# Kernel optimization log

Hardware: AMD Instinct MI355X
Metric: run time of the kernel (lower is better)

## Reference

```python
import math
import jax, jax.numpy as jnp
import numpy as np

B, T, D, H = 2, 2048, 768, 12
DH = D // H
EPS = 1e-5


def setup_inputs() -> dict:
    key = jax.random.key(0)
    ks = jax.random.split(key, 8)
    s = 0.02
    x = jax.random.normal(ks[0], (B, T, D), dtype=jnp.float32)
    lengths = jax.random.randint(ks[1], (B,), T // 2, T + 1)
    lengths = lengths.at[0].set(T)  # ensure max(lengths)==T (static shape)
    return {
        'x': x,
        'lengths': lengths,
        'w_qkv': jax.random.normal(ks[2], (D, 3 * D), dtype=jnp.float32) * s,
        'b_qkv': jnp.zeros((3 * D,), jnp.float32),
        'w_proj': jax.random.normal(ks[3], (D, D), dtype=jnp.float32) * s,
        'b_proj': jnp.zeros((D,), jnp.float32),
        'ln1_g': jnp.ones((D,), jnp.float32),
        'ln1_b': jnp.zeros((D,), jnp.float32),
        'w_fc': jax.random.normal(ks[4], (D, 4 * D), dtype=jnp.float32) * s,
        'b_fc': jnp.zeros((4 * D,), jnp.float32),
        'w_out': jax.random.normal(ks[5], (4 * D, D), dtype=jnp.float32) * s,
        'b_out': jnp.zeros((D,), jnp.float32),
        'ln2_g': jnp.ones((D,), jnp.float32),
        'ln2_b': jnp.zeros((D,), jnp.float32),
    }


def _gelu(x):
    c = math.sqrt(2.0 / math.pi)
    return 0.5 * x * (1.0 + jnp.tanh(c * (x + 0.044715 * x * x * x)))


def _layernorm(x, g, b):
    mu = jnp.mean(x, axis=-1, keepdims=True)
    var = jnp.mean(jnp.square(x - mu), axis=-1, keepdims=True)
    return (x - mu) * jax.lax.rsqrt(var + EPS) * g + b


def _block(x, lengths, w_qkv, b_qkv, w_proj, b_proj, ln1_g, ln1_b,
           w_fc, b_fc, w_out, b_out, ln2_g, ln2_b):
    dt = x.dtype
    # [B, T] validity mask from ragged lengths
    pos = jnp.arange(T)
    mask = (pos[None, :] < lengths[:, None]).astype(dt)

    # --- SeqMultiHeadAttention (scale=False) ---
    qkv = x @ w_qkv + b_qkv  # [B, T, 3D]
    q, k, v = jnp.split(qkv, 3, axis=-1)

    def split_heads(t):  # [B,T,D] -> [B,H,T,DH]
        return t.reshape(B, T, H, DH).transpose(0, 2, 1, 3)

    q, k, v = split_heads(q), split_heads(k), split_heads(v)
    w = jnp.einsum('bhqd,bhkd->bhqk', q, k)  # [B,H,T,T]
    amask = (mask[:, None, :, None] * mask[:, None, None, :])  # [B,1,T,T]
    w = w * amask + (-1e9) * (1.0 - amask)
    w = jax.nn.softmax(w, axis=-1) * amask
    a = jnp.einsum('bhqk,bhkd->bhqd', w, v)  # [B,H,T,DH]
    a = a.transpose(0, 2, 1, 3).reshape(B, T, D)
    a = a @ w_proj + b_proj

    # --- SeqLayerNorm 1: pack/unpack == per-position LN, padding zeroed ---
    n = _layernorm(x + a, ln1_g, ln1_b) * mask[..., None]

    # --- MLP (gelu) ---
    m = _gelu(n @ w_fc + b_fc) @ w_out + b_out

    # --- SeqLayerNorm 2 ---
    h = _layernorm(n + m, ln2_g, ln2_b) * mask[..., None]
    return h


def reference(x, lengths, w_qkv, b_qkv, w_proj, b_proj, ln1_g, ln1_b,
              w_fc, b_fc, w_out, b_out, ln2_g, ln2_b):
    return _block(x, lengths, w_qkv, b_qkv, w_proj, b_proj, ln1_g, ln1_b,
                  w_fc, b_fc, w_out, b_out, ln2_g, ln2_b)
```

## Files before the change

### kernel.cpp

```cpp
#include <hip/hip_runtime.h>
#include <hip/hip_bf16.h>
#include <math.h>

constexpr int Bc  = 2;
constexpr int Tc  = 2048;
constexpr int Dc  = 768;
constexpr int Hc  = 12;
constexpr int DHc = 64;
constexpr int M_ROWS = Bc * Tc;
constexpr int D3  = 3 * Dc;
constexpr int D4  = 4 * Dc;

typedef __attribute__((ext_vector_type(8))) short short8;
typedef __attribute__((ext_vector_type(4))) float f32x4;

__device__ __forceinline__ unsigned short f2bf(float v) {
    union { __hip_bfloat16 b; unsigned short u; } cv;
    cv.b = __float2bfloat16(v);
    return cv.u;
}
__device__ __forceinline__ float bf2f(unsigned short u) {
    union { __hip_bfloat16 b; unsigned short u; } cv;
    cv.u = u;
    return __bfloat162float(cv.b);
}
__device__ __forceinline__ void bsplit(float v, unsigned short& h, unsigned short& l) {
    h = f2bf(v);
    l = f2bf(v - bf2f(h));
}

__device__ __forceinline__ float gelu_f(float x) {
    const float c = 0.79788456080286535588f;
    return 0.5f * x * (1.0f + tanhf(c * (x + 0.044715f * x * x * x)));
}

__device__ __forceinline__ void glds16(const unsigned short* g, unsigned short* l) {
    __builtin_amdgcn_global_load_lds(
        (const __attribute__((address_space(1))) void*)g,
        (__attribute__((address_space(3))) void*)l, 16, 0, 0);
}

__device__ __forceinline__ void tcast8(
    const float* __restrict__ w, int ldw,
    unsigned short* __restrict__ th, int K, int N, int idx)
{
    const int n  = idx % N;
    const int k0 = (idx / N) * 8;
    unsigned short hv[8];
#pragma unroll
    for (int j = 0; j < 8; ++j)
        hv[j] = f2bf(w[(size_t)(k0 + j) * ldw + n]);
    const size_t o = (size_t)n * K + k0;
    *(ushort4*)(th + o)     = make_ushort4(hv[0], hv[1], hv[2], hv[3]);
    *(ushort4*)(th + o + 4) = make_ushort4(hv[4], hv[5], hv[6], hv[7]);
}

__global__ __launch_bounds__(256) void prepare_kernel(
    const float* __restrict__ x,
    const float* __restrict__ w_qkv, const float* __restrict__ w_proj,
    const float* __restrict__ w_fc,  const float* __restrict__ w_out,
    unsigned short* __restrict__ xh,
    unsigned short* __restrict__ wqkvT, unsigned short* __restrict__ wprojT,
    unsigned short* __restrict__ wfcT,  unsigned short* __restrict__ woutT)
{
    int id = blockIdx.x * 256 + threadIdx.x;
    if (id < 786432) {
        const float4 v = *(const float4*)(x + (size_t)id * 4);
        *(ushort4*)(xh + (size_t)id * 4) =
            make_ushort4(f2bf(v.x), f2bf(v.y), f2bf(v.z), f2bf(v.w));
        return;
    }
    id -= 786432;
    if (id < 221184) { tcast8(w_qkv, D3, wqkvT, Dc, D3, id); return; }
    id -= 221184;
    if (id < 73728)  { tcast8(w_proj, Dc, wprojT, Dc, Dc, id); return; }
    id -= 73728;
    if (id < 294912) { tcast8(w_fc, D4, wfcT, Dc, D4, id); return; }
    id -= 294912;
    tcast8(w_out, Dc, woutT, D4, Dc, id);
}

template <int TM, int MODE>
__global__ __launch_bounds__(256) void gemm_bf16(
    const unsigned short* __restrict__ A,
    const unsigned short* __restrict__ B,
    const float* __restrict__ bias,
    float* __restrict__ C, unsigned short* __restrict__ Cb,
    int M, int N, int K)
{
    constexpr int MT = TM / 32;
    __shared__ unsigned short Ash[TM * 64];
    __shared__ unsigned short Bsh[128 * 64];

    const int tid  = threadIdx.x;
    const int n0   = blockIdx.x * 128;
    const int m0   = blockIdx.y * TM;
    const int wave = tid >> 6;
    const int lane = tid & 63;
    const int wm   = (wave >> 1) * (TM / 2);
    const int wn   = (wave & 1) * 64;
    const int lrow = lane & 15;
    const int quad = lane >> 4;
    const int swz  = lrow & 7;

    f32x4 acc[MT][4];
    const f32x4 zero = {0.f, 0.f, 0.f, 0.f};
#pragma unroll
    for (int i = 0; i < MT; ++i)
#pragma unroll
        for (int j = 0; j < 4; ++j) acc[i][j] = zero;

    const int l8r  = lane >> 3;
    const int csel = ((lane & 7) ^ l8r) * 8;

    for (int ks = 0; ks < K; ks += 64) {
        __syncthreads();
#pragma unroll
        for (int j = 0; j < TM / 32; ++j) {
            const int rbase = wave * (TM / 4) + j * 8;
            const size_t g = (size_t)(m0 + rbase + l8r) * K + ks + csel;
            glds16(A + g, &Ash[rbase * 64]);
        }
#pragma unroll
        for (int j = 0; j < 4; ++j) {
            const int rbase = wave * 32 + j * 8;
            const size_t g = (size_t)(n0 + rbase + l8r) * K + ks + csel;
            glds16(B + g, &Bsh[rbase * 64]);
        }
        __syncthreads();

#pragma unroll
        for (int kk = 0; kk < 2; ++kk) {
            short8 fa[MT], fb[4];
            const int cl = kk * 4 + quad;
            const int pc = (cl ^ swz) * 8;
#pragma unroll
            for (int t = 0; t < MT; ++t)
                fa[t] = *(const short8*)&Ash[(wm + t * 16 + lrow) * 64 + pc];
#pragma unroll
            for (int t = 0; t < 4; ++t)
                fb[t] = *(const short8*)&Bsh[(wn + t * 16 + lrow) * 64 + pc];
#pragma unroll
            for (int mt = 0; mt < MT; ++mt)
#pragma unroll
                for (int nt = 0; nt < 4; ++nt)
                    acc[mt][nt] = __builtin_amdgcn_mfma_f32_16x16x32_bf16(
                        fa[mt], fb[nt], acc[mt][nt], 0, 0, 0);
        }
    }

#pragma unroll
    for (int mt = 0; mt < MT; ++mt) {
        const int rowb = m0 + wm + mt * 16 + quad * 4;
#pragma unroll
        for (int nt = 0; nt < 4; ++nt) {
            const int col = n0 + wn + nt * 16 + lrow;
            const float bv = bias[col];
#pragma unroll
            for (int r = 0; r < 4; ++r) {
                const size_t ci = (size_t)(rowb + r) * N + col;
                if (MODE == 0) {
                    C[ci] = acc[mt][nt][r] + bv;
                } else if (MODE == 1) {
                    Cb[ci] = f2bf(gelu_f(acc[mt][nt][r] + bv));
                } else {
                    Cb[ci] = f2bf(acc[mt][nt][r] + bv);
                }
            }
        }
    }
}

constexpr int KS  = 72;
constexpr int PS2 = 72;

__global__ __launch_bounds__(256) void flash_attn_bf16(
    const unsigned short* __restrict__ qkv,
    const int* __restrict__ lengths,
    unsigned short* __restrict__ oh)
{
    __shared__ unsigned short Kh[64 * KS];
    __shared__ unsigned short Vt[64 * KS];
    __shared__ unsigned short PfU[64 * PS2];

    const int tid  = threadIdx.x;
    const int wave = tid >> 6;
    const int lane = tid & 63;
    const int m    = lane & 15;
    const int quad = lane >> 4;

    const int nqt = Tc / 64;
    const int qt  = blockIdx.x % nqt;
    const int bh  = blockIdx.x / nqt;
    const int hh  = bh % Hc;
    const int b   = bh / Hc;
    const int len = lengths[b];
    const int q0  = qt * 64;
    const size_t rs = (size_t)D3;
    const unsigned short* base = qkv + (size_t)b * Tc * rs;
    const int qcol = hh * DHc;
    const int kcol = Dc + hh * DHc;
    const int vcol = 2 * Dc + hh * DHc;

    if (q0 >= len) {
#pragma unroll
        for (int r = 0; r < 4; ++r) {
            const int qrow = q0 + wave * 16 + quad * 4 + r;
            const size_t ob = (size_t)(b * Tc + qrow) * Dc + hh * DHc + m;
#pragma unroll
            for (int nt = 0; nt < 4; ++nt) oh[ob + nt * 16] = 0;
        }
        return;
    }

    const int ktEnd = (min(len, Tc) + 63) >> 6;

    short8 Qf[2];
#pragma unroll
    for (int ch = 0; ch < 2; ++ch) {
        const size_t ga = (size_t)(q0 + wave * 16 + m) * rs + qcol + ch * 32 + quad * 8;
        const short8 q8 = *(const short8*)&base[ga];
        short8 qs;
#pragma unroll
        for (int j = 0; j < 8; ++j)
            qs[j] = (short)f2bf(bf2f((unsigned short)q8[j]) * 1.44269504088896f);
        Qf[ch] = qs;
    }

    f32x4 Oacc[4];
    const f32x4 zero = {0.f, 0.f, 0.f, 0.f};
#pragma unroll
    for (int nt = 0; nt < 4; ++nt) Oacc[nt] = zero;
    float lrow[4] = {0.f, 0.f, 0.f, 0.f};

    const int kr0 = tid >> 3,          kc0 = (tid & 7) * 8;
    const int kr1 = (tid + 256) >> 3,  kc1 = ((tid + 256) & 7) * 8;
    const int pk  = (tid >> 4) * 4;
    const int pd  = (tid & 15) * 4;
    const int vswz = ((pk >> 3) ^ ((pd >> 2) & 7)) * 8 + (pk & 7);

    short8  pK0, pK1;
    ushort4 pV0, pV1, pV2, pV3;
    {
        pK0 = *(const short8*)&base[(size_t)kr0 * rs + kcol + kc0];
        pK1 = *(const short8*)&base[(size_t)kr1 * rs + kcol + kc1];
        pV0 = *(const ushort4*)&base[(size_t)(pk + 0) * rs + vcol + pd];
        pV1 = *(const ushort4*)&base[(size_t)(pk + 1) * rs + vcol + pd];
        pV2 = *(const ushort4*)&base[(size_t)(pk + 2) * rs + vcol + pd];
        pV3 = *(const ushort4*)&base[(size_t)(pk + 3) * rs + vcol + pd];
    }

    for (int kt = 0; kt < ktEnd; ++kt) {
        const int kbase = kt * 64;
        __syncthreads();

        *(short8*)&Kh[kr0 * KS + kc0] = pK0;
        *(short8*)&Kh[kr1 * KS + kc1] = pK1;
        *(ushort4*)&Vt[(pd + 0) * KS + vswz] = make_ushort4(pV0.x, pV1.x, pV2.x, pV3.x);
        *(ushort4*)&Vt[(pd + 1) * KS + vswz] = make_ushort4(pV0.y, pV1.y, pV2.y, pV3.y);
        *(ushort4*)&Vt[(pd + 2) * KS + vswz] = make_ushort4(pV0.z, pV1.z, pV2.z, pV3.z);
        *(ushort4*)&Vt[(pd + 3) * KS + vswz] = make_ushort4(pV0.w, pV1.w, pV2.w, pV3.w);
        __syncthreads();

        if (kt + 1 < ktEnd) {
            const int nb = kbase + 64;
            pK0 = *(const short8*)&base[(size_t)(nb + kr0) * rs + kcol + kc0];
            pK1 = *(const short8*)&base[(size_t)(nb + kr1) * rs + kcol + kc1];
            pV0 = *(const ushort4*)&base[(size_t)(nb + pk + 0) * rs + vcol + pd];
            pV1 = *(const ushort4*)&base[(size_t)(nb + pk + 1) * rs + vcol + pd];
            pV2 = *(const ushort4*)&base[(size_t)(nb + pk + 2) * rs + vcol + pd];
            pV3 = *(const ushort4*)&base[(size_t)(nb + pk + 3) * rs + vcol + pd];
        }

        f32x4 S4[4];
#pragma unroll
        for (int nt = 0; nt < 4; ++nt) S4[nt] = zero;
#pragma unroll
        for (int ch = 0; ch < 2; ++ch)
#pragma unroll
            for (int nt = 0; nt < 4; ++nt) {
                const short8 k8 = *(const short8*)&Kh[(nt * 16 + m) * KS + ch * 32 + quad * 8];
                S4[nt] = __builtin_amdgcn_mfma_f32_16x16x32_bf16(Qf[ch], k8, S4[nt], 0, 0, 0);
            }

        if (kbase + 64 > len) {
#pragma unroll
            for (int nt = 0; nt < 4; ++nt)
                if (kbase + nt * 16 + m >= len) {
#pragma unroll
                    for (int r = 0; r < 4; ++r) S4[nt][r] = -1e30f;
                }
        }

#pragma unroll
        for (int nt = 0; nt < 4; ++nt)
#pragma unroll
            for (int r = 0; r < 4; ++r) {
                const float p = __builtin_amdgcn_exp2f(S4[nt][r]);
                lrow[r] += p;
                PfU[(wave * 16 + quad * 4 + r) * PS2 + nt * 16 + m] = f2bf(p);
            }

#pragma unroll
        for (int ch = 0; ch < 2; ++ch) {
            const short8 P8 = *(const short8*)&PfU[(wave * 16 + m) * PS2 + ch * 32 + quad * 8];
#pragma unroll
            for (int nt = 0; nt < 4; ++nt) {
                const int pchunk = ((ch * 4 + quad) ^ ((nt * 4 + (m >> 2)) & 7)) * 8;
                const short8 v8 = *(const short8*)&Vt[(nt * 16 + m) * KS + pchunk];
                Oacc[nt] = __builtin_amdgcn_mfma_f32_16x16x32_bf16(P8, v8, Oacc[nt], 0, 0, 0);
            }
        }
    }

#pragma unroll
    for (int r = 0; r < 4; ++r) {
#pragma unroll
        for (int sh = 8; sh >= 1; sh >>= 1)
            lrow[r] += __shfl_xor(lrow[r], sh);
    }

#pragma unroll
    for (int r = 0; r < 4; ++r) {
        const int qrow = q0 + wave * 16 + quad * 4 + r;
        const size_t ob = (size_t)(b * Tc + qrow) * Dc + hh * DHc + m;
        if (qrow < len) {
            const float inv = 1.0f / lrow[r];
#pragma unroll
            for (int nt = 0; nt < 4; ++nt)
                oh[ob + nt * 16] = f2bf(Oacc[nt][r] * inv);
        } else {
#pragma unroll
            for (int nt = 0; nt < 4; ++nt)
                oh[ob + nt * 16] = 0;
        }
    }
}

__global__ __launch_bounds__(256) void ln_split_kernel(
    const float* __restrict__ X, const float* __restrict__ Y,
    const float* __restrict__ g, const float* __restrict__ beta,
    const int* __restrict__ lengths,
    unsigned short* __restrict__ outh, unsigned short* __restrict__ outl)
{
    __shared__ float red[4];
    const int row = blockIdx.x;
    const int b = row / Tc, t = row % Tc;
    const int len = lengths[b];
    const size_t basei = (size_t)row * Dc;
    const int tid = threadIdx.x;

    if (t >= len) {
        for (int j = tid; j < Dc; j += 256) { outh[basei + j] = 0; outl[basei + j] = 0; }
        return;
    }

    float v[3];
    float s = 0.f;
#pragma unroll
    for (int j = 0; j < 3; ++j) {
        int idx = tid + j * 256;
        v[j] = X[basei + idx] + Y[basei + idx];
        s += v[j];
    }
    const int lane = tid % 64, wid = tid / 64;
#pragma unroll
    for (int sh = 32; sh >= 1; sh >>= 1) s += __shfl_xor(s, sh);
    if (lane == 0) red[wid] = s;
    __syncthreads();
    s = red[0] + red[1] + red[2] + red[3];
    const float mu = s * (1.0f / Dc);

    float vs = 0.f;
#pragma unroll
    for (int j = 0; j < 3; ++j) { float dv = v[j] - mu; vs += dv * dv; }
    __syncthreads();
#pragma unroll
    for (int sh = 32; sh >= 1; sh >>= 1) vs += __shfl_xor(vs, sh);
    if (lane == 0) red[wid] = vs;
    __syncthreads();
    vs = red[0] + red[1] + red[2] + red[3];
    const float rstd = rsqrtf(vs * (1.0f / Dc) + 1e-5f);

#pragma unroll
    for (int j = 0; j < 3; ++j) {
        int idx = tid + j * 256;
        const float ov = (v[j] - mu) * rstd * g[idx] + beta[idx];
        unsigned short hh, ll;
        bsplit(ov, hh, ll);
        outh[basei + idx] = hh;
        outl[basei + idx] = ll;
    }
}

__global__ __launch_bounds__(256) void ln2_kernel(
    const unsigned short* __restrict__ Xh, const unsigned short* __restrict__ Xl,
    const float* Y,
    const float* __restrict__ g, const float* __restrict__ beta,
    const int* __restrict__ lengths, float* out)
{
    __shared__ float red[4];
    const int row = blockIdx.x;
    const int b = row / Tc, t = row % Tc;
    const int len = lengths[b];
    const size_t basei = (size_t)row * Dc;
    const int tid = threadIdx.x;

    if (t >= len) {
        for (int j = tid; j < Dc; j += 256) out[basei + j] = 0.f;
        return;
    }

    float v[3];
    float s = 0.f;
#pragma unroll
    for (int j = 0; j < 3; ++j) {
        int idx = tid + j * 256;
        v[j] = bf2f(Xh[basei + idx]) + bf2f(Xl[basei + idx]) + Y[basei + idx];
        s += v[j];
    }
    const int lane = tid % 64, wid = tid / 64;
#pragma unroll
    for (int sh = 32; sh >= 1; sh >>= 1) s += __shfl_xor(s, sh);
    if (lane == 0) red[wid] = s;
    __syncthreads();
    s = red[0] + red[1] + red[2] + red[3];
    const float mu = s * (1.0f / Dc);

    float vs = 0.f;
#pragma unroll
    for (int j = 0; j < 3; ++j) { float dv = v[j] - mu; vs += dv * dv; }
    __syncthreads();
#pragma unroll
    for (int sh = 32; sh >= 1; sh >>= 1) vs += __shfl_xor(vs, sh);
    if (lane == 0) red[wid] = vs;
    __syncthreads();
    vs = red[0] + red[1] + red[2] + red[3];
    const float rstd = rsqrtf(vs * (1.0f / Dc) + 1e-5f);

#pragma unroll
    for (int j = 0; j < 3; ++j) {
        int idx = tid + j * 256;
        out[basei + idx] = (v[j] - mu) * rstd * g[idx] + beta[idx];
    }
}

extern "C" void kernel_launch(void* const* d_in, const int* in_sizes, int n_in,
                              void* d_out, int out_size, void* d_ws, size_t ws_size,
                              hipStream_t stream)
{
    const float* x      = (const float*)d_in[0];
    const int*   lens   = (const int*)  d_in[1];
    const float* w_qkv  = (const float*)d_in[2];
    const float* b_qkv  = (const float*)d_in[3];
    const float* w_proj = (const float*)d_in[4];
    const float* b_proj = (const float*)d_in[5];
    const float* ln1_g  = (const float*)d_in[6];
    const float* ln1_b  = (const float*)d_in[7];
    const float* w_fc   = (const float*)d_in[8];
    const float* b_fc   = (const float*)d_in[9];
    const float* w_out  = (const float*)d_in[10];
    const float* b_out  = (const float*)d_in[11];
    const float* ln2_g  = (const float*)d_in[12];
    const float* ln2_b  = (const float*)d_in[13];

    if (ws_size < 51904512) return;

    char* ws = (char*)d_ws;
    unsigned short* qkvh  = (unsigned short*)(ws + 0);
    unsigned short* xh    = (unsigned short*)(ws + 18874368);
    unsigned short* ah    = xh;
    float*          projo = (float*)(ws + 0);
    unsigned short* fH    = (unsigned short*)(ws + 0);
    unsigned short* nh    = (unsigned short*)(ws + 25165824);
    unsigned short* nl    = (unsigned short*)(ws + 31457280);
    unsigned short* wqkvT = (unsigned short*)(ws + 37748736);
    unsigned short* wprojT= (unsigned short*)(ws + 41287680);
    unsigned short* wfcT  = (unsigned short*)(ws + 42467328);
    unsigned short* woutT = (unsigned short*)(ws + 47185920);
    float*          mbuf  = (float*)d_out;

    const dim3 blk(256);

    prepare_kernel<<<dim3(6528), blk, 0, stream>>>(
        x, w_qkv, w_proj, w_fc, w_out, xh, wqkvT, wprojT, wfcT, woutT);

    gemm_bf16<128, 3><<<dim3(D3 / 128, M_ROWS / 128), blk, 0, stream>>>(
        xh, wqkvT, b_qkv, nullptr, qkvh, M_ROWS, D3, Dc);

    flash_attn_bf16<<<dim3(Bc * Hc * (Tc / 64)), blk, 0, stream>>>(qkvh, lens, ah);

    gemm_bf16<64, 0><<<dim3(Dc / 128, M_ROWS / 64), blk, 0, stream>>>(
        ah, wprojT, b_proj, projo, nullptr, M_ROWS, Dc, Dc);

    ln_split_kernel<<<dim3(M_ROWS), blk, 0, stream>>>(x, projo, ln1_g, ln1_b, lens, nh, nl);

    gemm_bf16<128, 1><<<dim3(D4 / 128, M_ROWS / 128), blk, 0, stream>>>(
        nh, wfcT, b_fc, nullptr, fH, M_ROWS, D4, Dc);

    gemm_bf16<64, 0><<<dim3(Dc / 128, M_ROWS / 64), blk, 0, stream>>>(
        fH, woutT, b_out, mbuf, nullptr, M_ROWS, Dc, D4);

    ln2_kernel<<<dim3(M_ROWS), blk, 0, stream>>>(nh, nl, mbuf, ln2_g, ln2_b, lens,
                                                 (float*)d_out);
}
```

Measured before the change: 313.0 us.

## Double-buffer LDS tiles in bf16 GEMM to overlap global loads with MFMA

The bf16 GEMM kernel now keeps two LDS buffers for the A and B tiles. It issues the direct global-to-LDS loads for the next K step before running the MFMAs on the current buffer, with one barrier per iteration instead of two. The goal is to hide global memory latency behind matrix-core work. In exchange, shared memory use per block doubles, which can lower occupancy. Correctness also depends on the barrier waiting for the outstanding LDS-targeted loads.

```diff
diff --git a/kernel.cpp b/kernel.cpp
--- a/kernel.cpp
+++ b/kernel.cpp
@@ -89,8 +89,8 @@
     int M, int N, int K)
 {
     constexpr int MT = TM / 32;
-    __shared__ unsigned short Ash[TM * 64];
-    __shared__ unsigned short Bsh[128 * 64];
+    __shared__ unsigned short Ash[2][TM * 64];
+    __shared__ unsigned short Bsh[2][128 * 64];
 
     const int tid  = threadIdx.x;
     const int n0   = blockIdx.x * 128;
@@ -113,21 +113,38 @@
     const int l8r  = lane >> 3;
     const int csel = ((lane & 7) ^ l8r) * 8;
 
-    for (int ks = 0; ks < K; ks += 64) {
-        __syncthreads();
-#pragma unroll
-        for (int j = 0; j < TM / 32; ++j) {
-            const int rbase = wave * (TM / 4) + j * 8;
-            const size_t g = (size_t)(m0 + rbase + l8r) * K + ks + csel;
-            glds16(A + g, &Ash[rbase * 64]);
-        }
-#pragma unroll
-        for (int j = 0; j < 4; ++j) {
-            const int rbase = wave * 32 + j * 8;
-            const size_t g = (size_t)(n0 + rbase + l8r) * K + ks + csel;
-            glds16(B + g, &Bsh[rbase * 64]);
-        }
-        __syncthreads();
+    const int nsteps = K >> 6;
+
+#pragma unroll
+    for (int j = 0; j < TM / 32; ++j) {
+        const int rbase = wave * (TM / 4) + j * 8;
+        glds16(A + (size_t)(m0 + rbase + l8r) * K + csel, &Ash[0][rbase * 64]);
+    }
+#pragma unroll
+    for (int j = 0; j < 4; ++j) {
+        const int rbase = wave * 32 + j * 8;
+        glds16(B + (size_t)(n0 + rbase + l8r) * K + csel, &Bsh[0][rbase * 64]);
+    }
+    asm volatile("s_waitcnt vmcnt(0)" ::: "memory");
+    __syncthreads();
+
+    int cur = 0;
+    for (int s = 0; s < nsteps; ++s) {
+        if (s + 1 < nsteps) {
+            const int ksn = (s + 1) << 6;
+#pragma unroll
+            for (int j = 0; j < TM / 32; ++j) {
+                const int rbase = wave * (TM / 4) + j * 8;
+                glds16(A + (size_t)(m0 + rbase + l8r) * K + ksn + csel,
+                       &Ash[cur ^ 1][rbase * 64]);
+            }
+#pragma unroll
+            for (int j = 0; j < 4; ++j) {
+                const int rbase = wave * 32 + j * 8;
+                glds16(B + (size_t)(n0 + rbase + l8r) * K + ksn + csel,
+                       &Bsh[cur ^ 1][rbase * 64]);
+            }
+        }
 
 #pragma unroll
         for (int kk = 0; kk < 2; ++kk) {
@@ -136,10 +153,10 @@
             const int pc = (cl ^ swz) * 8;
 #pragma unroll
             for (int t = 0; t < MT; ++t)
-                fa[t] = *(const short8*)&Ash[(wm + t * 16 + lrow) * 64 + pc];
+                fa[t] = *(const short8*)&Ash[cur][(wm + t * 16 + lrow) * 64 + pc];
 #pragma unroll
             for (int t = 0; t < 4; ++t)
-                fb[t] = *(const short8*)&Bsh[(wn + t * 16 + lrow) * 64 + pc];
+                fb[t] = *(const short8*)&Bsh[cur][(wn + t * 16 + lrow) * 64 + pc];
 #pragma unroll
             for (int mt = 0; mt < MT; ++mt)
 #pragma unroll
@@ -147,6 +164,9 @@
                     acc[mt][nt] = __builtin_amdgcn_mfma_f32_16x16x32_bf16(
                         fa[mt], fb[nt], acc[mt][nt], 0, 0, 0);
         }
+
+        __syncthreads();
+        cur ^= 1;
     }
 
 #pragma unroll
```

Result: slower. 327.6 us (+4.7%).

## Add 256x256 double-buffered bf16 GEMM for QKV and FC projections

Applied to the files above, without the earlier changes.

Introduces a new 512-thread GEMM kernel with 256x256 output tiles, double-buffered LDS staging via direct global-to-LDS loads, an XOR-swizzled shared layout and an XCD-aware block index remap. It replaces the 128x128 GEMM for the QKV and FC1 (GELU) projections. The aim is more operand reuse per tile, overlap of loads with MFMA work, and better L2 locality per XCD. In exchange it uses 128KB of LDS and large accumulator register arrays, which limits occupancy. The grids are small (144 and 192 blocks on a 256-CU device), which may leave CUs idle.

```diff
diff --git a/kernel.cpp b/kernel.cpp
--- a/kernel.cpp
+++ b/kernel.cpp
@@ -78,6 +78,111 @@
     if (id < 294912) { tcast8(w_fc, D4, wfcT, Dc, D4, id); return; }
     id -= 294912;
     tcast8(w_out, Dc, woutT, D4, Dc, id);
+}
+
+template <int MODE>
+__global__ __launch_bounds__(512) void gemm256_bf16(
+    const unsigned short* __restrict__ A,
+    const unsigned short* __restrict__ B,
+    const float* __restrict__ bias,
+    float* __restrict__ C, unsigned short* __restrict__ Cb,
+    int N, int K)
+{
+    __shared__ unsigned short Ash[2][256 * 64];
+    __shared__ unsigned short Bsh[2][256 * 64];
+
+    const int tid  = threadIdx.x;
+    const int wave = tid >> 6;
+    const int lane = tid & 63;
+
+    const int nper = gridDim.x >> 3;
+    const int gid  = (blockIdx.x & 7) * nper + (blockIdx.x >> 3);
+    const int bx   = gid / 16;
+    const int by   = gid % 16;
+    const int m0 = by * 256, n0 = bx * 256;
+
+    const int wm   = (wave >> 2) * 128;
+    const int wn   = (wave & 3) * 64;
+    const int lrow = lane & 15;
+    const int quad = lane >> 4;
+    const int swz  = lrow & 7;
+
+    f32x4 acc[8][4];
+    const f32x4 zero = {0.f, 0.f, 0.f, 0.f};
+#pragma unroll
+    for (int i = 0; i < 8; ++i)
+#pragma unroll
+        for (int j = 0; j < 4; ++j) acc[i][j] = zero;
+
+    const int l8r  = lane >> 3;
+    const int csel = ((lane & 7) ^ l8r) * 8;
+
+    const int nsteps = K >> 6;
+
+    auto stage = [&](int t, int b) {
+        const int ks = t << 6;
+#pragma unroll
+        for (int j = 0; j < 4; ++j) {
+            const int rbase = wave * 32 + j * 8;
+            glds16(A + (size_t)(m0 + rbase + l8r) * K + ks + csel,
+                   &Ash[b][rbase * 64]);
+        }
+#pragma unroll
+        for (int j = 0; j < 4; ++j) {
+            const int rbase = wave * 32 + j * 8;
+            glds16(B + (size_t)(n0 + rbase + l8r) * K + ks + csel,
+                   &Bsh[b][rbase * 64]);
+        }
+    };
+
+    stage(0, 0);
+    __syncthreads();
+
+    int cur = 0;
+    for (int s = 0; s < nsteps; ++s) {
+        if (s + 1 < nsteps) stage(s + 1, cur ^ 1);
+
+#pragma unroll
+        for (int kk = 0; kk < 2; ++kk) {
+            const int pc = ((kk * 4 + quad) ^ swz) * 8;
+            short8 fb[4];
+#pragma unroll
+            for (int nt = 0; nt < 4; ++nt)
+                fb[nt] = *(const short8*)&Bsh[cur][(wn + nt * 16 + lrow) * 64 + pc];
+#pragma unroll
+            for (int mt = 0; mt < 8; ++mt) {
+                const short8 fa = *(const short8*)&Ash[cur][(wm + mt * 16 + lrow) * 64 + pc];
+#pragma unroll
+                for (int nt = 0; nt < 4; ++nt)
+                    acc[mt][nt] = __builtin_amdgcn_mfma_f32_16x16x32_bf16(
+                        fa, fb[nt], acc[mt][nt], 0, 0, 0);
+            }
+        }
+
+        __syncthreads();
+        cur ^= 1;
+    }
+
+#pragma unroll
+    for (int mt = 0; mt < 8; ++mt) {
+        const int rowb = m0 + wm + mt * 16 + quad * 4;
+#pragma unroll
+        for (int nt = 0; nt < 4; ++nt) {
+            const int col = n0 + wn + nt * 16 + lrow;
+            const float bv = bias[col];
+#pragma unroll
+            for (int r = 0; r < 4; ++r) {
+                const size_t ci = (size_t)(rowb + r) * N + col;
+                if (MODE == 0) {
+                    C[ci] = acc[mt][nt][r] + bv;
+                } else if (MODE == 1) {
+                    Cb[ci] = f2bf(gelu_f(acc[mt][nt][r] + bv));
+                } else {
+                    Cb[ci] = f2bf(acc[mt][nt][r] + bv);
+                }
+            }
+        }
+    }
 }
 
 template <int TM, int MODE>
@@ -485,8 +590,8 @@
     prepare_kernel<<<dim3(6528), blk, 0, stream>>>(
         x, w_qkv, w_proj, w_fc, w_out, xh, wqkvT, wprojT, wfcT, woutT);
 
-    gemm_bf16<128, 3><<<dim3(D3 / 128, M_ROWS / 128), blk, 0, stream>>>(
-        xh, wqkvT, b_qkv, nullptr, qkvh, M_ROWS, D3, Dc);
+    gemm256_bf16<3><<<dim3((D3 / 256) * 16), dim3(512), 0, stream>>>(
+        xh, wqkvT, b_qkv, nullptr, qkvh, D3, Dc);
 
     flash_attn_bf16<<<dim3(Bc * Hc * (Tc / 64)), blk, 0, stream>>>(qkvh, lens, ah);
 
@@ -495,8 +600,8 @@
 
     ln_split_kernel<<<dim3(M_ROWS), blk, 0, stream>>>(x, projo, ln1_g, ln1_b, lens, nh, nl);
 
-    gemm_bf16<128, 1><<<dim3(D4 / 128, M_ROWS / 128), blk, 0, stream>>>(
-        nh, wfcT, b_fc, nullptr, fH, M_ROWS, D4, Dc);
+    gemm256_bf16<1><<<dim3((D4 / 256) * 16), dim3(512), 0, stream>>>(
+        nh, wfcT, b_fc, nullptr, fH, D4, Dc);
 
     gemm_bf16<64, 0><<<dim3(Dc / 128, M_ROWS / 64), blk, 0, stream>>>(
         fH, woutT, b_out, mbuf, nullptr, M_ROWS, Dc, D4);
```

Result: slower. 323.4 us (+3.3%).

## Split attention over key range into two halves and combine partials

Applied to the files above, without the earlier changes.

The attention kernel now splits the key-tile loop into two halves run by separate blocks. Each block writes an unnormalized fp32 partial output and a row sum, and a new combine kernel adds them and normalizes to bf16. The goal is twice the grid parallelism on a GPU with many CUs, at the cost of extra fp32 global traffic and one more launch. The softmax appears to use a fixed max (no running max), which is what makes plain summing of the partials valid. The QKV and FC GEMMs also move to 64-row tiles for more blocks.

```diff
diff --git a/kernel.cpp b/kernel.cpp
--- a/kernel.cpp
+++ b/kernel.cpp
@@ -10,6 +10,7 @@
 constexpr int M_ROWS = Bc * Tc;
 constexpr int D3  = 3 * Dc;
 constexpr int D4  = 4 * Dc;
+constexpr int HT  = Bc * Hc * Tc;
 
 typedef __attribute__((ext_vector_type(8))) short short8;
 typedef __attribute__((ext_vector_type(4))) float f32x4;
@@ -174,10 +175,11 @@
 constexpr int KS  = 72;
 constexpr int PS2 = 72;
 
-__global__ __launch_bounds__(256) void flash_attn_bf16(
+__global__ __launch_bounds__(256) void flash_attn_split(
     const unsigned short* __restrict__ qkv,
     const int* __restrict__ lengths,
-    unsigned short* __restrict__ oh)
+    float* __restrict__ O0, float* __restrict__ O1,
+    float* __restrict__ lp)
 {
     __shared__ unsigned short Kh[64 * KS];
     __shared__ unsigned short Vt[64 * KS];
@@ -189,9 +191,12 @@
     const int m    = lane & 15;
     const int quad = lane >> 4;
 
-    const int nqt = Tc / 64;
-    const int qt  = blockIdx.x % nqt;
-    const int bh  = blockIdx.x / nqt;
+    const int nqt  = Tc / 64;
+    const int nblk = Bc * Hc * nqt;
+    const int half = blockIdx.x / nblk;
+    const int bid  = blockIdx.x % nblk;
+    const int qt  = bid % nqt;
+    const int bh  = bid / nqt;
     const int hh  = bh % Hc;
     const int b   = bh / Hc;
     const int len = lengths[b];
@@ -202,18 +207,24 @@
     const int kcol = Dc + hh * DHc;
     const int vcol = 2 * Dc + hh * DHc;
 
+    float* __restrict__ Op = half ? O1 : O0;
+    const int lbase = half * HT + (b * Hc + hh) * Tc;
+
     if (q0 >= len) {
 #pragma unroll
         for (int r = 0; r < 4; ++r) {
             const int qrow = q0 + wave * 16 + quad * 4 + r;
             const size_t ob = (size_t)(b * Tc + qrow) * Dc + hh * DHc + m;
 #pragma unroll
-            for (int nt = 0; nt < 4; ++nt) oh[ob + nt * 16] = 0;
+            for (int nt = 0; nt < 4; ++nt) Op[ob + nt * 16] = 0.f;
+            if (m == 0) lp[lbase + qrow] = 0.f;
         }
         return;
     }
 
     const int ktEnd = (min(len, Tc) + 63) >> 6;
+    const int kt0 = (half * ktEnd) >> 1;
+    const int kt1 = ((half + 1) * ktEnd) >> 1;
 
     short8 Qf[2];
 #pragma unroll
@@ -242,15 +253,16 @@
     short8  pK0, pK1;
     ushort4 pV0, pV1, pV2, pV3;
     {
-        pK0 = *(const short8*)&base[(size_t)kr0 * rs + kcol + kc0];
-        pK1 = *(const short8*)&base[(size_t)kr1 * rs + kcol + kc1];
-        pV0 = *(const ushort4*)&base[(size_t)(pk + 0) * rs + vcol + pd];
-        pV1 = *(const ushort4*)&base[(size_t)(pk + 1) * rs + vcol + pd];
-        pV2 = *(const ushort4*)&base[(size_t)(pk + 2) * rs + vcol + pd];
-        pV3 = *(const ushort4*)&base[(size_t)(pk + 3) * rs + vcol + pd];
-    }
-
-    for (int kt = 0; kt < ktEnd; ++kt) {
+        const int nb = kt0 * 64;
+        pK0 = *(const short8*)&base[(size_t)(nb + kr0) * rs + kcol + kc0];
+        pK1 = *(const short8*)&base[(size_t)(nb + kr1) * rs + kcol + kc1];
+        pV0 = *(const ushort4*)&base[(size_t)(nb + pk + 0) * rs + vcol + pd];
+        pV1 = *(const ushort4*)&base[(size_t)(nb + pk + 1) * rs + vcol + pd];
+        pV2 = *(const ushort4*)&base[(size_t)(nb + pk + 2) * rs + vcol + pd];
+        pV3 = *(const ushort4*)&base[(size_t)(nb + pk + 3) * rs + vcol + pd];
+    }
+
+    for (int kt = kt0; kt < kt1; ++kt) {
         const int kbase = kt * 64;
         __syncthreads();
 
@@ -262,7 +274,7 @@
         *(ushort4*)&Vt[(pd + 3) * KS + vswz] = make_ushort4(pV0.w, pV1.w, pV2.w, pV3.w);
         __syncthreads();
 
-        if (kt + 1 < ktEnd) {
+        if (kt + 1 < kt1) {
             const int nb = kbase + 64;
             pK0 = *(const short8*)&base[(size_t)(nb + kr0) * rs + kcol + kc0];
             pK1 = *(const short8*)&base[(size_t)(nb + kr1) * rs + kcol + kc1];
@@ -325,15 +337,35 @@
         const int qrow = q0 + wave * 16 + quad * 4 + r;
         const size_t ob = (size_t)(b * Tc + qrow) * Dc + hh * DHc + m;
         if (qrow < len) {
-            const float inv = 1.0f / lrow[r];
 #pragma unroll
             for (int nt = 0; nt < 4; ++nt)
-                oh[ob + nt * 16] = f2bf(Oacc[nt][r] * inv);
+                Op[ob + nt * 16] = Oacc[nt][r];
+            if (m == 0) lp[lbase + qrow] = lrow[r];
         } else {
 #pragma unroll
             for (int nt = 0; nt < 4; ++nt)
-                oh[ob + nt * 16] = 0;
-        }
+                Op[ob + nt * 16] = 0.f;
+            if (m == 0) lp[lbase + qrow] = 0.f;
+        }
+    }
+}
+
+__global__ __launch_bounds__(256) void attn_combine(
+    const float* __restrict__ O0, const float* __restrict__ O1,
+    const float* __restrict__ lp,
+    unsigned short* __restrict__ ah)
+{
+    const int row = blockIdx.x;
+    const int b = row / Tc, t = row % Tc;
+    const int tid = threadIdx.x;
+    const size_t basei = (size_t)row * Dc;
+#pragma unroll
+    for (int j = 0; j < 3; ++j) {
+        const int col = tid + j * 256;
+        const int h = col >> 6;
+        const float l = lp[(b * Hc + h) * Tc + t] + lp[HT + (b * Hc + h) * Tc + t];
+        const float o = O0[basei + col] + O1[basei + col];
+        ah[basei + col] = (l > 0.f) ? f2bf(o / l) : (unsigned short)0;
     }
 }
 
@@ -480,22 +512,29 @@
     unsigned short* woutT = (unsigned short*)(ws + 47185920);
     float*          mbuf  = (float*)d_out;
 
+    float* O0 = (float*)d_out;
+    float* O1 = (float*)(ws + 25165824);
+    float* lp = (float*)(ws + 37748736);
+
     const dim3 blk(256);
 
     prepare_kernel<<<dim3(6528), blk, 0, stream>>>(
         x, w_qkv, w_proj, w_fc, w_out, xh, wqkvT, wprojT, wfcT, woutT);
 
-    gemm_bf16<128, 3><<<dim3(D3 / 128, M_ROWS / 128), blk, 0, stream>>>(
+    gemm_bf16<64, 3><<<dim3(D3 / 128, M_ROWS / 64), blk, 0, stream>>>(
         xh, wqkvT, b_qkv, nullptr, qkvh, M_ROWS, D3, Dc);
 
-    flash_attn_bf16<<<dim3(Bc * Hc * (Tc / 64)), blk, 0, stream>>>(qkvh, lens, ah);
+    flash_attn_split<<<dim3(2 * Bc * Hc * (Tc / 64)), blk, 0, stream>>>(
+        qkvh, lens, O0, O1, lp);
+
+    attn_combine<<<dim3(M_ROWS), blk, 0, stream>>>(O0, O1, lp, ah);
 
     gemm_bf16<64, 0><<<dim3(Dc / 128, M_ROWS / 64), blk, 0, stream>>>(
         ah, wprojT, b_proj, projo, nullptr, M_ROWS, Dc, Dc);
 
     ln_split_kernel<<<dim3(M_ROWS), blk, 0, stream>>>(x, projo, ln1_g, ln1_b, lens, nh, nl);
 
-    gemm_bf16<128, 1><<<dim3(D4 / 128, M_ROWS / 128), blk, 0, stream>>>(
+    gemm_bf16<64, 1><<<dim3(D4 / 128, M_ROWS / 64), blk, 0, stream>>>(
         nh, wfcT, b_fc, nullptr, fH, M_ROWS, D4, Dc);
 
     gemm_bf16<64, 0><<<dim3(Dc / 128, M_ROWS / 64), blk, 0, stream>>>(
```

Result: slower. 326.6 us (+4.3%).
